# Optimization experiments

Hardware: AMD Instinct MI355X
Metric: run time of the kernel (lower is better)

Reference implementation:

```python
import jax, jax.numpy as jnp
import numpy as np

D_MODEL = 1024
N_HEADS = 16
D_HEAD = D_MODEL // N_HEADS


def setup_inputs() -> dict:
    key = jax.random.key(0)
    k_x, k_qkv, k_proj = jax.random.split(key, 3)
    x = jax.random.normal(k_x, (4, 2048, D_MODEL), dtype=jnp.float32)
    # nn.Linear(d_model, 3*d_model, bias=False): weight shape [3*d_model, d_model]
    scale = 1.0 / np.sqrt(D_MODEL)
    W_qkv = jax.random.uniform(k_qkv, (3 * D_MODEL, D_MODEL), dtype=jnp.float32, minval=-scale, maxval=scale)
    W_proj = jax.random.uniform(k_proj, (D_MODEL, D_MODEL), dtype=jnp.float32, minval=-scale, maxval=scale)
    return {"x": x, "W_qkv": W_qkv, "W_proj": W_proj}


def reference(x, W_qkv, W_proj):
    B, T, C = x.shape
    qkv = jnp.einsum('btc,fc->btf', x, W_qkv)  # [B,T,3C]
    q, k, v = jnp.split(qkv, 3, axis=-1)
    # [B,T,H,Dh] -> [B,H,T,Dh]
    q = q.reshape(B, T, N_HEADS, D_HEAD).transpose(0, 2, 1, 3)
    k = k.reshape(B, T, N_HEADS, D_HEAD).transpose(0, 2, 1, 3)
    v = v.reshape(B, T, N_HEADS, D_HEAD).transpose(0, 2, 1, 3)
    att = jnp.einsum('bhqd,bhkd->bhqk', q, k) / jnp.sqrt(jnp.float32(D_HEAD))
    att = jax.nn.softmax(att, axis=-1)
    y = jnp.einsum('bhqk,bhkd->bhqd', att, v)
    y = y.transpose(0, 2, 1, 3).reshape(B, T, C)
    return jnp.einsum('btc,oc->bto', y, W_proj)
```

## Files before the change

### kernel.cpp

```cpp
#include <hip/hip_runtime.h>
#include <stdint.h>
#include <stddef.h>

#define SEQ   2048
#define NH    16
#define DH    64
#define DM    1024
#define NTOK  8192

typedef unsigned short u16;
typedef unsigned int u32;
typedef short bf16x8 __attribute__((ext_vector_type(8)));
typedef float f32x4  __attribute__((ext_vector_type(4)));
typedef unsigned short u16x4 __attribute__((ext_vector_type(4)));
typedef unsigned short u16x8 __attribute__((ext_vector_type(8)));

#define QSCALE 0.18033688011112042f

#define WAIT_VM12 0x0F7C
#define WAIT_VM4  0x0F74
#define WAIT_VM0  0x0F70

__device__ __forceinline__ u16 f2bf(float f) {
  union { float f; unsigned u; } v; v.f = f;
  return (u16)((v.u + 0x7FFFu + ((v.u >> 16) & 1u)) >> 16);
}

__device__ __forceinline__ void gload_lds16(const void* g, void* l) {
  __builtin_amdgcn_global_load_lds(
      (const __attribute__((address_space(1))) void*)g,
      (__attribute__((address_space(3))) void*)l, 16, 0, 0);
}

__global__ __launch_bounds__(256) void cast_kernel(const float* __restrict__ src,
                                                   u16* __restrict__ dst, int n4) {
  int i = blockIdx.x * 256 + threadIdx.x;
  if (i < n4) {
    const float4 f = ((const float4*)src)[i];
    u16x4 o;
    o.x = f2bf(f.x); o.y = f2bf(f.y); o.z = f2bf(f.z); o.w = f2bf(f.w);
    ((u16x4*)dst)[i] = o;
  }
}

__global__ __launch_bounds__(256) void pack_b(const float* __restrict__ W,
                                              u16* __restrict__ Bp, int NS) {
  const int chunk = blockIdx.x * 256 + threadIdx.x;
  const int lane = chunk & 63, blk = chunk >> 6;
  const int c = blk / NS, s = blk % NS;
  const int n = s * 16 + (lane & 15);
  const int k0 = c * 32 + (lane >> 4) * 8;
  const float4 f0 = *(const float4*)&W[(size_t)n * DM + k0];
  const float4 f1 = *(const float4*)&W[(size_t)n * DM + k0 + 4];
  u16x8 o;
  o[0] = f2bf(f0.x); o[1] = f2bf(f0.y); o[2] = f2bf(f0.z); o[3] = f2bf(f0.w);
  o[4] = f2bf(f1.x); o[5] = f2bf(f1.y); o[6] = f2bf(f1.z); o[7] = f2bf(f1.w);
  *(u16x8*)&Bp[(size_t)chunk * 8] = o;
}

template <int EPI>
__global__ __launch_bounds__(256) void gemm_flat(
    const u16* __restrict__ A, const u16* __restrict__ Bp, int NS, int N_,
    u16* __restrict__ Qo, u16* __restrict__ Ko, u16* __restrict__ Vto,
    float* __restrict__ Co) {
  __shared__ __align__(16) u16 sA[2][128 * 64];
  const int tid = threadIdx.x;
  const int wave = tid >> 6, lane = tid & 63;
  const int l16 = lane & 15, quad = lane >> 4;
  const int sw = l16 & 7;
  const int wm = (wave >> 1) * 64, wn = (wave & 1) * 64;
  const int row0 = blockIdx.y * 128, col0 = blockIdx.x * 128;
  const int ck0 = ((quad ^ sw) << 3);
  const int ck1 = (((quad + 4) ^ sw) << 3);
  const int scol = (col0 + wn) >> 4;
  const u16* bpw = Bp + (size_t)lane * 8;

  f32x4 acc[4][4];
  for (int a = 0; a < 4; ++a)
    for (int b = 0; b < 4; ++b) acc[a][b] = (f32x4){0.f, 0.f, 0.f, 0.f};

  bf16x8 bfr[2][2][4];

  for (int j = 0; j < 4; ++j) {
    const int li = j * 256 + tid;
    const int r = li >> 3;
    const int cs = (((li & 7) ^ (r & 7)) << 3);
    gload_lds16(A + (size_t)(row0 + r) * DM + cs, (char*)sA[0] + li * 16);
  }
  for (int kk = 0; kk < 2; ++kk) {
    const u16* bb = bpw + ((size_t)kk * NS + scol) * 512;
    for (int i = 0; i < 4; ++i)
      bfr[0][kk][i] = *(const bf16x8*)(bb + i * 512);
  }

#pragma unroll 2
  for (int t = 0; t < 16; ++t) {
    const int cur = t & 1;
    const int tn = (t + 1) & 15;
    const int k1 = tn << 6;
    for (int j = 0; j < 4; ++j) {
      const int li = j * 256 + tid;
      const int r = li >> 3;
      const int cs = (((li & 7) ^ (r & 7)) << 3);
      gload_lds16(A + (size_t)(row0 + r) * DM + k1 + cs, (char*)sA[cur ^ 1] + li * 16);
    }
    for (int kk = 0; kk < 2; ++kk) {
      const u16* bb = bpw + ((size_t)(tn * 2 + kk) * NS + scol) * 512;
      for (int i = 0; i < 4; ++i)
        bfr[cur ^ 1][kk][i] = *(const bf16x8*)(bb + i * 512);
    }
    __builtin_amdgcn_s_waitcnt(WAIT_VM12);
    __builtin_amdgcn_s_barrier();
    const u16* sa = sA[cur];
    for (int kk = 0; kk < 2; ++kk) {
      const int cko = kk ? ck1 : ck0;
      bf16x8 af[4];
      for (int i = 0; i < 4; ++i)
        af[i] = *(const bf16x8*)&sa[(wm + i * 16 + l16) * 64 + cko];
      for (int mi = 0; mi < 4; ++mi)
        for (int ni = 0; ni < 4; ++ni)
          acc[mi][ni] = __builtin_amdgcn_mfma_f32_16x16x32_bf16(
              af[mi], bfr[cur][kk][ni], acc[mi][ni], 0, 0, 0);
    }
    __builtin_amdgcn_s_barrier();
  }
  __builtin_amdgcn_s_waitcnt(WAIT_VM0);

  if (EPI == 0) {
    const int which = col0 >> 10;
    for (int mi = 0; mi < 4; ++mi)
      for (int ni = 0; ni < 4; ++ni) {
        const int rowb = row0 + wm + mi * 16 + quad * 4;
        const int col = col0 + wn + ni * 16 + l16;
        const int b = rowb >> 11, t = rowb & (SEQ - 1);
        const int c = col & (DM - 1);
        const int h = c >> 6, d = c & 63;
        const size_t bh = (size_t)b * NH + h;
        if (which == 2) {
          u16x4 pk;
          pk.x = f2bf(acc[mi][ni][0]); pk.y = f2bf(acc[mi][ni][1]);
          pk.z = f2bf(acc[mi][ni][2]); pk.w = f2bf(acc[mi][ni][3]);
          *(u16x4*)&Vto[(bh * DH + d) * SEQ + t] = pk;
        } else {
          for (int r = 0; r < 4; ++r) {
            const float v = acc[mi][ni][r];
            if (which == 0) Qo[(bh * SEQ + t + r) * DH + d] = f2bf(v * QSCALE);
            else            Ko[(bh * SEQ + t + r) * DH + d] = f2bf(v);
          }
        }
      }
  } else {
    for (int mi = 0; mi < 4; ++mi)
      for (int ni = 0; ni < 4; ++ni)
        for (int r = 0; r < 4; ++r) {
          const int row = row0 + wm + mi * 16 + quad * 4 + r;
          const int col = col0 + wn + ni * 16 + l16;
          Co[(size_t)row * N_ + col] = acc[mi][ni][r];
        }
  }
}

#define PSTRIDE 72
__global__ __launch_bounds__(256) void flash_attn(
    const u16* __restrict__ Q, const u16* __restrict__ Kk,
    const u16* __restrict__ Vt, u16* __restrict__ Y) {
  __shared__ __align__(16) u16 sK[2][64 * 64];
  __shared__ __align__(16) u16 sV[2][64 * 64];
  __shared__ __align__(16) u16 sP[4 * 64 * PSTRIDE];
  const int tid = threadIdx.x, wave = tid >> 6, lane = tid & 63;
  const int l16 = lane & 15, quad = lane >> 4;
  const int sw = l16 & 7;
  const int ck0 = ((quad ^ sw) << 3);
  const int ck1 = (((quad + 4) ^ sw) << 3);
  const int rloc = tid >> 3;
  const int cs = (((tid & 7) ^ (rloc & 7)) << 3);
  const int bh = blockIdx.y;
  const int q0 = blockIdx.x * 256 + wave * 64;
  const size_t qkBase = (size_t)bh * SEQ * DH;
  const size_t vtBase = (size_t)bh * DH * SEQ;

  bf16x8 qf[4][2];
  for (int ms = 0; ms < 4; ++ms) {
    const u16* qrow = Q + qkBase + (size_t)(q0 + ms * 16 + l16) * DH;
    qf[ms][0] = *(const bf16x8*)(qrow + quad * 8);
    qf[ms][1] = *(const bf16x8*)(qrow + 32 + quad * 8);
  }

  bf16x8 onesf;
  for (int i = 0; i < 8; ++i) onesf[i] = (short)0x3F80;

  f32x4 o[4][4];
  f32x4 osum[4];
  for (int a = 0; a < 4; ++a) {
    osum[a] = (f32x4){0.f, 0.f, 0.f, 0.f};
    for (int b = 0; b < 4; ++b) o[a][b] = (f32x4){0.f, 0.f, 0.f, 0.f};
  }

  u16* myP = sP + wave * 64 * PSTRIDE;

  for (int j = 0; j < 2; ++j) {
    const int r = j * 32 + rloc;
    gload_lds16(Kk + qkBase + (size_t)r * DH + cs, (char*)sK[0] + (j * 256 + tid) * 16);
    gload_lds16(Vt + vtBase + (size_t)r * SEQ + cs, (char*)sV[0] + (j * 256 + tid) * 16);
  }
  for (int t = 0; t < 32; ++t) {
    const int cur = t & 1;
    const int kt1 = ((t + 1) & 31) * 64;
    for (int j = 0; j < 2; ++j) {
      const int r = j * 32 + rloc;
      gload_lds16(Kk + qkBase + (size_t)(kt1 + r) * DH + cs, (char*)sK[cur ^ 1] + (j * 256 + tid) * 16);
      gload_lds16(Vt + vtBase + (size_t)r * SEQ + kt1 + cs, (char*)sV[cur ^ 1] + (j * 256 + tid) * 16);
    }
    __builtin_amdgcn_s_waitcnt(WAIT_VM4);
    __builtin_amdgcn_s_barrier();
    const u16* sk = sK[cur];
    const u16* sv = sV[cur];

    for (int nt = 0; nt < 4; ++nt) {
      bf16x8 kf0 = *(const bf16x8*)&sk[(nt * 16 + l16) * 64 + ck0];
      bf16x8 kf1 = *(const bf16x8*)&sk[(nt * 16 + l16) * 64 + ck1];
      for (int ms = 0; ms < 4; ++ms) {
        f32x4 st = (f32x4){0.f, 0.f, 0.f, 0.f};
        st = __builtin_amdgcn_mfma_f32_16x16x32_bf16(kf0, qf[ms][0], st, 0, 0, 0);
        st = __builtin_amdgcn_mfma_f32_16x16x32_bf16(kf1, qf[ms][1], st, 0, 0, 0);
        const u32 u0 = __builtin_bit_cast(u32, __builtin_amdgcn_exp2f(st[0]));
        const u32 u1 = __builtin_bit_cast(u32, __builtin_amdgcn_exp2f(st[1]));
        const u32 u2 = __builtin_bit_cast(u32, __builtin_amdgcn_exp2f(st[2]));
        const u32 u3 = __builtin_bit_cast(u32, __builtin_amdgcn_exp2f(st[3]));
        uint2 pk;
        pk.x = __builtin_amdgcn_perm(u1, u0, 0x07060302u);
        pk.y = __builtin_amdgcn_perm(u3, u2, 0x07060302u);
        *(uint2*)&myP[(ms * 16 + l16) * PSTRIDE + nt * 16 + quad * 4] = pk;
      }
    }

    bf16x8 pf[4][2];
    for (int ms = 0; ms < 4; ++ms) {
      pf[ms][0] = *(const bf16x8*)&myP[(ms * 16 + l16) * PSTRIDE + quad * 8];
      pf[ms][1] = *(const bf16x8*)&myP[(ms * 16 + l16) * PSTRIDE + 32 + quad * 8];
    }
    for (int ms = 0; ms < 4; ++ms) {
      osum[ms] = __builtin_amdgcn_mfma_f32_16x16x32_bf16(pf[ms][0], onesf, osum[ms], 0, 0, 0);
      osum[ms] = __builtin_amdgcn_mfma_f32_16x16x32_bf16(pf[ms][1], onesf, osum[ms], 0, 0, 0);
    }
    for (int ds = 0; ds < 4; ++ds) {
      bf16x8 vf0 = *(const bf16x8*)&sv[(ds * 16 + l16) * 64 + ck0];
      bf16x8 vf1 = *(const bf16x8*)&sv[(ds * 16 + l16) * 64 + ck1];
      for (int ms = 0; ms < 4; ++ms) {
        o[ms][ds] = __builtin_amdgcn_mfma_f32_16x16x32_bf16(pf[ms][0], vf0, o[ms][ds], 0, 0, 0);
        o[ms][ds] = __builtin_amdgcn_mfma_f32_16x16x32_bf16(pf[ms][1], vf1, o[ms][ds], 0, 0, 0);
      }
    }
    __builtin_amdgcn_s_barrier();
  }
  __builtin_amdgcn_s_waitcnt(WAIT_VM0);

  float rl[4][4];
  for (int ms = 0; ms < 4; ++ms)
    for (int r = 0; r < 4; ++r)
      rl[ms][r] = __frcp_rn(osum[ms][r]);

  const int b = bh >> 4, h = bh & (NH - 1);
  for (int ms = 0; ms < 4; ++ms)
    for (int ds = 0; ds < 4; ++ds)
      for (int r = 0; r < 4; ++r) {
        const int t = q0 + ms * 16 + quad * 4 + r;
        const int d = ds * 16 + l16;
        Y[((size_t)(b * SEQ + t)) * DM + h * DH + d] = f2bf(o[ms][ds][r] * rl[ms][r]);
      }
}

extern "C" void kernel_launch(void* const* d_in, const int* in_sizes, int n_in,
                              void* d_out, int out_size, void* d_ws, size_t ws_size,
                              hipStream_t stream) {
  const float* x     = (const float*)d_in[0];
  const float* Wqkv  = (const float*)d_in[1];
  const float* Wproj = (const float*)d_in[2];
  float* out = (float*)d_out;

  u16* xb     = (u16*)d_ws;
  u16* bpQkv  = xb + (size_t)NTOK * DM;
  u16* bpProj = bpQkv + (size_t)3 * DM * DM;
  u16* Qb  = bpProj + (size_t)DM * DM;
  u16* Kb  = Qb + (size_t)NTOK * DM;
  u16* Vtb = Kb + (size_t)NTOK * DM;
  u16* Yb  = Vtb + (size_t)NTOK * DM;

  {
    int n4 = NTOK * DM / 4;
    cast_kernel<<<(n4 + 255) / 256, 256, 0, stream>>>(x, xb, n4);
    pack_b<<<3 * DM * DM / 8 / 256, 256, 0, stream>>>(Wqkv, bpQkv, 3 * DM / 16);
    pack_b<<<DM * DM / 8 / 256, 256, 0, stream>>>(Wproj, bpProj, DM / 16);
  }

  gemm_flat<0><<<dim3(3 * DM / 128, NTOK / 128), 256, 0, stream>>>(
      xb, bpQkv, 3 * DM / 16, 3 * DM, Qb, Kb, Vtb, nullptr);

  flash_attn<<<dim3(SEQ / 256, 4 * NH), 256, 0, stream>>>(Qb, Kb, Vtb, Yb);

  gemm_flat<1><<<dim3(DM / 128, NTOK / 128), 256, 0, stream>>>(
      Yb, bpProj, DM / 16, DM, nullptr, nullptr, nullptr, out);
}
```

Baseline: 283.1 us.

## Keep softmax probabilities in registers instead of round-tripping through LDS

```diff
diff --git a/kernel.cpp b/kernel.cpp
--- a/kernel.cpp
+++ b/kernel.cpp
@@ -11,9 +11,11 @@
 typedef unsigned short u16;
 typedef unsigned int u32;
 typedef short bf16x8 __attribute__((ext_vector_type(8)));
+typedef short bf16x4 __attribute__((ext_vector_type(4)));
 typedef float f32x4  __attribute__((ext_vector_type(4)));
 typedef unsigned short u16x4 __attribute__((ext_vector_type(4)));
 typedef unsigned short u16x8 __attribute__((ext_vector_type(8)));
+typedef unsigned int u32x4 __attribute__((ext_vector_type(4)));
 
 #define QSCALE 0.18033688011112042f
 
@@ -30,6 +32,13 @@
   __builtin_amdgcn_global_load_lds(
       (const __attribute__((address_space(1))) void*)g,
       (__attribute__((address_space(3))) void*)l, 16, 0, 0);
+}
+
+__device__ __forceinline__ bf16x8 cat44(bf16x4 a, bf16x4 b) {
+  bf16x8 r;
+  r[0] = a[0]; r[1] = a[1]; r[2] = a[2]; r[3] = a[3];
+  r[4] = b[0]; r[5] = b[1]; r[6] = b[2]; r[7] = b[3];
+  return r;
 }
 
 __global__ __launch_bounds__(256) void cast_kernel(const float* __restrict__ src,
@@ -160,13 +169,11 @@
   }
 }
 
-#define PSTRIDE 72
 __global__ __launch_bounds__(256) void flash_attn(
     const u16* __restrict__ Q, const u16* __restrict__ Kk,
     const u16* __restrict__ Vt, u16* __restrict__ Y) {
   __shared__ __align__(16) u16 sK[2][64 * 64];
   __shared__ __align__(16) u16 sV[2][64 * 64];
-  __shared__ __align__(16) u16 sP[4 * 64 * PSTRIDE];
   const int tid = threadIdx.x, wave = tid >> 6, lane = tid & 63;
   const int l16 = lane & 15, quad = lane >> 4;
   const int sw = l16 & 7;
@@ -179,6 +186,12 @@
   const size_t qkBase = (size_t)bh * SEQ * DH;
   const size_t vtBase = (size_t)bh * DH * SEQ;
 
+  const int q2 = quad >> 1, q1o = (quad & 1) << 2;
+  const int vA0 = (((q2 + 0) ^ sw) << 3) + q1o;
+  const int vB0 = (((q2 + 2) ^ sw) << 3) + q1o;
+  const int vA1 = (((q2 + 4) ^ sw) << 3) + q1o;
+  const int vB1 = (((q2 + 6) ^ sw) << 3) + q1o;
+
   bf16x8 qf[4][2];
   for (int ms = 0; ms < 4; ++ms) {
     const u16* qrow = Q + qkBase + (size_t)(q0 + ms * 16 + l16) * DH;
@@ -195,8 +208,6 @@
     osum[a] = (f32x4){0.f, 0.f, 0.f, 0.f};
     for (int b = 0; b < 4; ++b) o[a][b] = (f32x4){0.f, 0.f, 0.f, 0.f};
   }
-
-  u16* myP = sP + wave * 64 * PSTRIDE;
 
   for (int j = 0; j < 2; ++j) {
     const int r = j * 32 + rloc;
@@ -216,9 +227,12 @@
     const u16* sk = sK[cur];
     const u16* sv = sV[cur];
 
+    u32x4 pw[4][2];
+#pragma unroll
     for (int nt = 0; nt < 4; ++nt) {
-      bf16x8 kf0 = *(const bf16x8*)&sk[(nt * 16 + l16) * 64 + ck0];
-      bf16x8 kf1 = *(const bf16x8*)&sk[(nt * 16 + l16) * 64 + ck1];
+      const bf16x8 kf0 = *(const bf16x8*)&sk[(nt * 16 + l16) * 64 + ck0];
+      const bf16x8 kf1 = *(const bf16x8*)&sk[(nt * 16 + l16) * 64 + ck1];
+#pragma unroll
       for (int ms = 0; ms < 4; ++ms) {
         f32x4 st = (f32x4){0.f, 0.f, 0.f, 0.f};
         st = __builtin_amdgcn_mfma_f32_16x16x32_bf16(kf0, qf[ms][0], st, 0, 0, 0);
@@ -227,28 +241,34 @@
         const u32 u1 = __builtin_bit_cast(u32, __builtin_amdgcn_exp2f(st[1]));
         const u32 u2 = __builtin_bit_cast(u32, __builtin_amdgcn_exp2f(st[2]));
         const u32 u3 = __builtin_bit_cast(u32, __builtin_amdgcn_exp2f(st[3]));
-        uint2 pk;
-        pk.x = __builtin_amdgcn_perm(u1, u0, 0x07060302u);
-        pk.y = __builtin_amdgcn_perm(u3, u2, 0x07060302u);
-        *(uint2*)&myP[(ms * 16 + l16) * PSTRIDE + nt * 16 + quad * 4] = pk;
+        pw[ms][nt >> 1][(nt & 1) * 2]     = __builtin_amdgcn_perm(u1, u0, 0x07060302u);
+        pw[ms][nt >> 1][(nt & 1) * 2 + 1] = __builtin_amdgcn_perm(u3, u2, 0x07060302u);
       }
     }
 
-    bf16x8 pf[4][2];
+#pragma unroll
     for (int ms = 0; ms < 4; ++ms) {
-      pf[ms][0] = *(const bf16x8*)&myP[(ms * 16 + l16) * PSTRIDE + quad * 8];
-      pf[ms][1] = *(const bf16x8*)&myP[(ms * 16 + l16) * PSTRIDE + 32 + quad * 8];
-    }
-    for (int ms = 0; ms < 4; ++ms) {
-      osum[ms] = __builtin_amdgcn_mfma_f32_16x16x32_bf16(pf[ms][0], onesf, osum[ms], 0, 0, 0);
-      osum[ms] = __builtin_amdgcn_mfma_f32_16x16x32_bf16(pf[ms][1], onesf, osum[ms], 0, 0, 0);
-    }
+      osum[ms] = __builtin_amdgcn_mfma_f32_16x16x32_bf16(
+          __builtin_bit_cast(bf16x8, pw[ms][0]), onesf, osum[ms], 0, 0, 0);
+      osum[ms] = __builtin_amdgcn_mfma_f32_16x16x32_bf16(
+          __builtin_bit_cast(bf16x8, pw[ms][1]), onesf, osum[ms], 0, 0, 0);
+    }
+
+#pragma unroll
     for (int ds = 0; ds < 4; ++ds) {
-      bf16x8 vf0 = *(const bf16x8*)&sv[(ds * 16 + l16) * 64 + ck0];
-      bf16x8 vf1 = *(const bf16x8*)&sv[(ds * 16 + l16) * 64 + ck1];
+      const int rb = (ds * 16 + l16) * 64;
+      const bf16x4 a0 = *(const bf16x4*)&sv[rb + vA0];
+      const bf16x4 b0 = *(const bf16x4*)&sv[rb + vB0];
+      const bf16x4 a1 = *(const bf16x4*)&sv[rb + vA1];
+      const bf16x4 b1 = *(const bf16x4*)&sv[rb + vB1];
+      const bf16x8 vf0 = cat44(a0, b0);
+      const bf16x8 vf1 = cat44(a1, b1);
+#pragma unroll
       for (int ms = 0; ms < 4; ++ms) {
-        o[ms][ds] = __builtin_amdgcn_mfma_f32_16x16x32_bf16(pf[ms][0], vf0, o[ms][ds], 0, 0, 0);
-        o[ms][ds] = __builtin_amdgcn_mfma_f32_16x16x32_bf16(pf[ms][1], vf1, o[ms][ds], 0, 0, 0);
+        o[ms][ds] = __builtin_amdgcn_mfma_f32_16x16x32_bf16(
+            __builtin_bit_cast(bf16x8, pw[ms][0]), vf0, o[ms][ds], 0, 0, 0);
+        o[ms][ds] = __builtin_amdgcn_mfma_f32_16x16x32_bf16(
+            __builtin_bit_cast(bf16x8, pw[ms][1]), vf1, o[ms][ds], 0, 0, 0);
       }
     }
     __builtin_amdgcn_s_barrier();
```

Result: slower. 294.3 us (+3.9%).
